# Kernel optimization log

Measured on AMD Instinct MI355X. Metric: run time of the kernel, lower is better.

## Reference

```python
import jax, jax.numpy as jnp
import numpy as np
from jax import lax

NUM_GROUPS = 16
EPS = 1e-5
POOL = 4
CLAMP_MIN, CLAMP_MAX = 0.0, 1.0


def setup_inputs() -> dict:
    key = jax.random.key(0)
    k = jax.random.split(key, 6)
    x = jax.random.normal(k[0], (128, 8, 128, 128), dtype=jnp.float32)
    conv_w = jax.random.normal(k[1], (64, 8, 3, 3), dtype=jnp.float32) * 0.1
    conv_b = jax.random.normal(k[2], (64,), dtype=jnp.float32) * 0.1
    gn_w = jnp.ones((64,), dtype=jnp.float32) + 0.1 * jax.random.normal(k[3], (64,), dtype=jnp.float32)
    gn_b = 0.1 * jax.random.normal(k[4], (64,), dtype=jnp.float32)
    scale = jnp.ones((64, 1, 1), dtype=jnp.float32) + 0.1 * jax.random.normal(k[5], (64, 1, 1), dtype=jnp.float32)
    return {"x": x, "conv_w": conv_w, "conv_b": conv_b, "gn_w": gn_w, "gn_b": gn_b, "scale": scale}


def reference(x, conv_w, conv_b, gn_w, gn_b, scale):
    # Conv2d: stride 1, no padding -> [N, 64, 126, 126]
    y = lax.conv_general_dilated(
        x, conv_w, window_strides=(1, 1), padding="VALID",
        dimension_numbers=("NCHW", "OIHW", "NCHW"))
    y = y + conv_b[None, :, None, None]

    # GroupNorm over (C/G, H, W) per (N, group), biased variance, eps=1e-5
    N, C, H, W = y.shape
    yg = y.reshape(N, NUM_GROUPS, -1)
    mean = jnp.mean(yg, axis=-1, keepdims=True)
    var = jnp.mean(jnp.square(yg - mean), axis=-1, keepdims=True)
    yn = ((yg - mean) * lax.rsqrt(var + EPS)).reshape(N, C, H, W)
    yn = yn * gn_w[None, :, None, None] + gn_b[None, :, None, None]

    # Per-channel scale (scale has shape [C,1,1])
    yn = yn * scale[None]

    # MaxPool2d(kernel=4, stride=4) -> [N, 64, 31, 31]
    yp = lax.reduce_window(yn, -jnp.inf, lax.max,
                           window_dimensions=(1, 1, POOL, POOL),
                           window_strides=(1, 1, POOL, POOL),
                           padding="VALID")

    # Clamp
    return jnp.clip(yp, CLAMP_MIN, CLAMP_MAX)
```

## Files before the change

kernel.cpp:

```cpp
#include <hip/hip_runtime.h>
#include <math.h>

#define N_IMG 128
#define IC 8
#define IH 128
#define IW 128
#define OC 64
#define NG 16
#define PH 31
#define PW 31
#define GN_EPS 1e-5f
#define CSTR (IH * IW)
#define NBAND 4

typedef float f32x4 __attribute__((ext_vector_type(4)));
typedef short s16x8 __attribute__((ext_vector_type(8)));
typedef int   i32x4 __attribute__((ext_vector_type(4)));

__device__ __forceinline__ unsigned cvt_pk_bf16(float a, float b) {
    unsigned r;
    asm("v_cvt_pk_bf16_f32 %0, %1, %2" : "=v"(r) : "v"(a), "v"(b));
    return r;
}
__device__ __forceinline__ float bf16lo_f(unsigned p) { return __uint_as_float(p << 16); }
__device__ __forceinline__ float bf16hi_f(unsigned p) { return __uint_as_float(p & 0xFFFF0000u); }

__device__ __forceinline__ s16x8 mk_frag(unsigned a, unsigned b, unsigned c, unsigned d) {
    union { i32x4 i; s16x8 s; } u;
    u.i = (i32x4){(int)a, (int)b, (int)c, (int)d};
    return u.s;
}

__device__ __forceinline__ void split8(const float v[8], s16x8* hi, s16x8* lo) {
    unsigned h[4], l[4];
#pragma unroll
    for (int e = 0; e < 4; e++) {
        float a = v[2 * e], b = v[2 * e + 1];
        unsigned hp = cvt_pk_bf16(a, b);
        float ra = a - bf16lo_f(hp);
        float rb = b - bf16hi_f(hp);
        h[e] = hp;
        l[e] = cvt_pk_bf16(ra, rb);
    }
    *hi = mk_frag(h[0], h[1], h[2], h[3]);
    *lo = mk_frag(l[0], l[1], l[2], l[3]);
}

__attribute__((amdgpu_waves_per_eu(2, 4)))
__launch_bounds__(256)
__global__ void conv_pool_mfma_phase1(const float* __restrict__ x,
                                      const float* __restrict__ conv_w,
                                      const float* __restrict__ conv_b,
                                      const float* __restrict__ gn_w,
                                      const float* __restrict__ gn_b,
                                      const float* __restrict__ scale,
                                      float* __restrict__ out,
                                      float* __restrict__ ws) {
    const int b = blockIdx.x;
    const int wid = ((b & 7) << 6) | (b >> 3);
    const int n = wid >> 2;
    const int band = wid & 3;
    const int tid = threadIdx.x;
    const int lane = tid & 63;
    const int wave = tid >> 6;
    const int p15 = lane & 15;
    const int lg = lane >> 4;

    __shared__ float gsum[4][NG][2];

    const float* xn = x + (size_t)n * (IC * CSTR);

    int icA[6], khA[6], rowoffA[6];
#pragma unroll
    for (int sh = 0; sh < 6; sh++) {
        int s = sh >> 1, h = sh & 1;
        int k0 = 32 * s + 16 * h + 4 * lg;
        int ic = k0 / 12;
        int kk = k0 - 12 * ic;
        int kh = kk >> 2;
        icA[sh] = ic; khA[sh] = kh;
        rowoffA[sh] = ic * CSTR + kh * IW;
    }

    s16x8 Ah[4][3], Al[4][3];
#pragma unroll
    for (int q = 0; q < 4; q++) {
        int c = q * 16 + p15;
        float sg = (gn_w[c] * scale[c] >= 0.f) ? 1.f : -1.f;
#pragma unroll
        for (int s = 0; s < 3; s++) {
            float wf[8];
#pragma unroll
            for (int h = 0; h < 2; h++) {
                int sh = s * 2 + h;
                int ic = icA[sh], kh = khA[sh];
#pragma unroll
                for (int kw = 0; kw < 4; kw++)
                    wf[h * 4 + kw] = (kw < 3)
                        ? conv_w[c * (IC * 9) + ic * 9 + kh * 3 + kw] * sg
                        : 0.f;
            }
            split8(wf, &Ah[q][s], &Al[q][s]);
        }
    }

    float bias4[4][4], sgn4[4][4];
#pragma unroll
    for (int q = 0; q < 4; q++)
#pragma unroll
        for (int r = 0; r < 4; r++) {
            int c = q * 16 + 4 * lg + r;
            float sg = (gn_w[c] * scale[c] >= 0.f) ? 1.f : -1.f;
            sgn4[q][r] = sg;
            bias4[q][r] = conv_b[c] * sg;
        }

    float sA[4], ssA[4];
#pragma unroll
    for (int q = 0; q < 4; q++) { sA[q] = 0.f; ssA[q] = 0.f; }

    const int nc = (band < 3) ? 8 * PW : 7 * PW;
    const int phb = band * 8;
    const int pi = p15 >> 2, pj = p15 & 3;

#pragma unroll 1
    for (int cell = wave; cell < nc; cell += 4) {
        int lph = cell / 31;
        int pwc = cell - lph * 31;
        int ph = phb + lph;
        int posoff = (4 * ph + pi) * IW + 4 * pwc + pj;

        f32x4 acc[4];
#pragma unroll
        for (int q = 0; q < 4; q++)
            acc[q] = (f32x4){bias4[q][0], bias4[q][1], bias4[q][2], bias4[q][3]};

#pragma unroll
        for (int s = 0; s < 3; s++) {
            float bv[8];
#pragma unroll
            for (int h = 0; h < 2; h++) {
                const float* p = xn + rowoffA[s * 2 + h] + posoff;
                bv[h * 4 + 0] = p[0]; bv[h * 4 + 1] = p[1];
                bv[h * 4 + 2] = p[2]; bv[h * 4 + 3] = p[3];
            }
            s16x8 Bh, Bl;
            split8(bv, &Bh, &Bl);
#pragma unroll
            for (int q = 0; q < 4; q++) {
                acc[q] = __builtin_amdgcn_mfma_f32_16x16x32_bf16(Ah[q][s], Bh, acc[q], 0, 0, 0);
                acc[q] = __builtin_amdgcn_mfma_f32_16x16x32_bf16(Ah[q][s], Bl, acc[q], 0, 0, 0);
                acc[q] = __builtin_amdgcn_mfma_f32_16x16x32_bf16(Al[q][s], Bh, acc[q], 0, 0, 0);
            }
        }

#pragma unroll
        for (int q = 0; q < 4; q++) {
            float m0 = acc[q][0], m1 = acc[q][1], m2 = acc[q][2], m3 = acc[q][3];
            float sp = sgn4[q][0] * m0 + sgn4[q][1] * m1
                     + sgn4[q][2] * m2 + sgn4[q][3] * m3;
            float sq = m0 * m0 + m1 * m1 + m2 * m2 + m3 * m3;
#pragma unroll
            for (int o = 1; o < 16; o <<= 1) {
                sp += __shfl_xor(sp, o, 64);
                sq += __shfl_xor(sq, o, 64);
                m0 = fmaxf(m0, __shfl_xor(m0, o, 64));
                m1 = fmaxf(m1, __shfl_xor(m1, o, 64));
                m2 = fmaxf(m2, __shfl_xor(m2, o, 64));
                m3 = fmaxf(m3, __shfl_xor(m3, o, 64));
            }
            sA[q] += sp; ssA[q] += sq;
            if (p15 == 0) {
                int c = q * 16 + 4 * lg;
                size_t ob = (((size_t)n * OC + c) * PH + ph) * PW + pwc;
                out[ob] = m0;
                out[ob + PH * PW] = m1;
                out[ob + 2 * PH * PW] = m2;
                out[ob + 3 * PH * PW] = m3;
            }
        }
    }

#pragma unroll 1
    for (int t = 2 * wave; t < 2 * wave + 2; t++) {
        int eb = band * 8 + t;
        int posrow, poscol, valid;
        if (eb < 16) {
            posrow = 8 * eb + (p15 >> 1);
            poscol = 124 + (p15 & 1);
            valid = (posrow <= 125);
        } else {
            posrow = 124 + (p15 >> 3);
            poscol = 8 * (eb - 16) + (p15 & 7);
            valid = (poscol <= 123);
        }

        f32x4 acc[4];
#pragma unroll
        for (int q = 0; q < 4; q++)
            acc[q] = (f32x4){bias4[q][0], bias4[q][1], bias4[q][2], bias4[q][3]};

#pragma unroll
        for (int s = 0; s < 3; s++) {
            float bv[8];
#pragma unroll
            for (int h = 0; h < 2; h++) {
                int sh = s * 2 + h;
                int xr = posrow + khA[sh]; if (xr > 127) xr = 127;
                const float* p = xn + icA[sh] * CSTR + xr * IW;
                int c0 = poscol;
                int c1 = c0 + 1; if (c1 > 127) c1 = 127;
                int c2 = c0 + 2; if (c2 > 127) c2 = 127;
                int c3 = c0 + 3; if (c3 > 127) c3 = 127;
                bv[h * 4 + 0] = p[c0]; bv[h * 4 + 1] = p[c1];
                bv[h * 4 + 2] = p[c2]; bv[h * 4 + 3] = p[c3];
            }
            s16x8 Bh, Bl;
            split8(bv, &Bh, &Bl);
#pragma unroll
            for (int q = 0; q < 4; q++) {
                acc[q] = __builtin_amdgcn_mfma_f32_16x16x32_bf16(Ah[q][s], Bh, acc[q], 0, 0, 0);
                acc[q] = __builtin_amdgcn_mfma_f32_16x16x32_bf16(Ah[q][s], Bl, acc[q], 0, 0, 0);
                acc[q] = __builtin_amdgcn_mfma_f32_16x16x32_bf16(Al[q][s], Bh, acc[q], 0, 0, 0);
            }
        }

        float vmask = valid ? 1.f : 0.f;
#pragma unroll
        for (int q = 0; q < 4; q++) {
            float m0 = acc[q][0] * vmask, m1 = acc[q][1] * vmask;
            float m2 = acc[q][2] * vmask, m3 = acc[q][3] * vmask;
            float sp = sgn4[q][0] * m0 + sgn4[q][1] * m1
                     + sgn4[q][2] * m2 + sgn4[q][3] * m3;
            float sq = m0 * m0 + m1 * m1 + m2 * m2 + m3 * m3;
#pragma unroll
            for (int o = 1; o < 16; o <<= 1) {
                sp += __shfl_xor(sp, o, 64);
                sq += __shfl_xor(sq, o, 64);
            }
            sA[q] += sp; ssA[q] += sq;
        }
    }

    if (p15 == 0) {
#pragma unroll
        for (int q = 0; q < 4; q++) {
            gsum[wave][q * 4 + lg][0] = sA[q];
            gsum[wave][q * 4 + lg][1] = ssA[q];
        }
    }
    __syncthreads();
    if (tid < 32) {
        int g = tid >> 1, which = tid & 1;
        float v = gsum[0][g][which] + gsum[1][g][which]
                + gsum[2][g][which] + gsum[3][g][which];
        ws[((size_t)(n * NBAND + band) * NG + g) * 2 + which] = v;
    }
}

__launch_bounds__(256)
__global__ void finalize_phase2(const float* __restrict__ gn_w,
                                const float* __restrict__ gn_b,
                                const float* __restrict__ scale,
                                const float* __restrict__ ws,
                                float* __restrict__ out) {
    const int total = N_IMG * OC * PH * PW;
    const float inv_count = 1.f / (float)(4 * 126 * 126);
    int stride = gridDim.x * 256;
    for (int i = blockIdx.x * 256 + threadIdx.x; i < total; i += stride) {
        int n = i / (OC * PH * PW);
        int rem = i - n * (OC * PH * PW);
        int c = rem / (PH * PW);
        int g = c >> 2;
        float S = 0.f, SS = 0.f;
#pragma unroll
        for (int bnd = 0; bnd < NBAND; bnd++) {
            size_t wb = ((size_t)(n * NBAND + bnd) * NG + g) * 2;
            S += ws[wb];
            SS += ws[wb + 1];
        }
        float mean = S * inv_count;
        float var = SS * inv_count - mean * mean;
        if (var < 0.f) var = 0.f;
        float rstd = rsqrtf(var + GN_EPS);
        float gw = gn_w[c], sc = scale[c];
        float a2 = rstd * fabsf(gw * sc);
        float b2 = (gn_b[c] - mean * rstd * gw) * sc;
        float v = fmaf(a2, out[i], b2);
        out[i] = fminf(fmaxf(v, 0.f), 1.f);
    }
}

extern "C" void kernel_launch(void* const* d_in, const int* in_sizes, int n_in,
                              void* d_out, int out_size, void* d_ws, size_t ws_size,
                              hipStream_t stream) {
    const float* x      = (const float*)d_in[0];
    const float* conv_w = (const float*)d_in[1];
    const float* conv_b = (const float*)d_in[2];
    const float* gn_w   = (const float*)d_in[3];
    const float* gn_b   = (const float*)d_in[4];
    const float* scale  = (const float*)d_in[5];
    float* out = (float*)d_out;
    float* ws  = (float*)d_ws;

    hipLaunchKernelGGL(conv_pool_mfma_phase1, dim3(N_IMG * NBAND), dim3(256),
                       0, stream, x, conv_w, conv_b, gn_w, gn_b, scale, out, ws);
    hipLaunchKernelGGL(finalize_phase2, dim3(2048), dim3(256), 0, stream,
                       gn_w, gn_b, scale, ws, out);
}
```

Measured before the change: 328.9 us.

## Map MFMA columns to pool windows so max-pool reduces in registers

Result: slower. 449.7 us (+36.7%).

```diff
diff --git a/kernel.cpp b/kernel.cpp
--- a/kernel.cpp
+++ b/kernel.cpp
@@ -119,80 +119,100 @@
 #pragma unroll
     for (int q = 0; q < 4; q++) { sA[q] = 0.f; ssA[q] = 0.f; }
 
-    const int nc = (band < 3) ? 8 * PW : 7 * PW;
+    const int ntile = (band < 3) ? 16 : 14;
     const int phb = band * 8;
-    const int pi = p15 >> 2, pj = p15 & 3;
 
 #pragma unroll 1
-    for (int cell = wave; cell < nc; cell += 4) {
-        int lph = cell / 31;
-        int pwc = cell - lph * 31;
-        int ph = phb + lph;
-        int posoff = (4 * ph + pi) * IW + 4 * pwc + pj;
-
-        f32x4 acc[4];
+    for (int t = wave; t < ntile; t += 4) {
+        const int ph = phb + (t >> 1);
+        const int tb = (t & 1) * 16;
+        const int pw = tb + p15;
+        const int valid = (pw <= 30);
+        const int pwc = valid ? pw : 30;
+        const float msk = valid ? 1.f : 0.f;
+        const float* xtile = xn + (4 * ph) * IW + 4 * pwc;
+
+        f32x4 vmax[4];
 #pragma unroll
         for (int q = 0; q < 4; q++)
-            acc[q] = (f32x4){bias4[q][0], bias4[q][1], bias4[q][2], bias4[q][3]};
-
-#pragma unroll
-        for (int s = 0; s < 3; s++) {
-            float bv[8];
-#pragma unroll
-            for (int h = 0; h < 2; h++) {
-                const float* p = xn + rowoffA[s * 2 + h] + posoff;
-                bv[h * 4 + 0] = p[0]; bv[h * 4 + 1] = p[1];
-                bv[h * 4 + 2] = p[2]; bv[h * 4 + 3] = p[3];
-            }
-            s16x8 Bh, Bl;
-            split8(bv, &Bh, &Bl);
-#pragma unroll
-            for (int q = 0; q < 4; q++) {
-                acc[q] = __builtin_amdgcn_mfma_f32_16x16x32_bf16(Ah[q][s], Bh, acc[q], 0, 0, 0);
-                acc[q] = __builtin_amdgcn_mfma_f32_16x16x32_bf16(Ah[q][s], Bl, acc[q], 0, 0, 0);
-                acc[q] = __builtin_amdgcn_mfma_f32_16x16x32_bf16(Al[q][s], Bh, acc[q], 0, 0, 0);
-            }
-        }
-
-#pragma unroll
-        for (int q = 0; q < 4; q++) {
-            float m0 = acc[q][0], m1 = acc[q][1], m2 = acc[q][2], m3 = acc[q][3];
-            float sp = sgn4[q][0] * m0 + sgn4[q][1] * m1
-                     + sgn4[q][2] * m2 + sgn4[q][3] * m3;
-            float sq = m0 * m0 + m1 * m1 + m2 * m2 + m3 * m3;
-#pragma unroll
-            for (int o = 1; o < 16; o <<= 1) {
-                sp += __shfl_xor(sp, o, 64);
-                sq += __shfl_xor(sq, o, 64);
-                m0 = fmaxf(m0, __shfl_xor(m0, o, 64));
-                m1 = fmaxf(m1, __shfl_xor(m1, o, 64));
-                m2 = fmaxf(m2, __shfl_xor(m2, o, 64));
-                m3 = fmaxf(m3, __shfl_xor(m3, o, 64));
-            }
-            sA[q] += sp; ssA[q] += sq;
-            if (p15 == 0) {
-                int c = q * 16 + 4 * lg;
-                size_t ob = (((size_t)n * OC + c) * PH + ph) * PW + pwc;
-                out[ob] = m0;
-                out[ob + PH * PW] = m1;
-                out[ob + 2 * PH * PW] = m2;
-                out[ob + 3 * PH * PW] = m3;
-            }
+            vmax[q] = (f32x4){-INFINITY, -INFINITY, -INFINITY, -INFINITY};
+
+#pragma unroll
+        for (int pi = 0; pi < 4; pi++) {
+            float row8[6][8];
+#pragma unroll
+            for (int sh = 0; sh < 6; sh++) {
+                const float* p = xtile + rowoffA[sh] + pi * IW;
+                float4 a = *(const float4*)p;
+                float4 bq = *(const float4*)(p + 4);
+                row8[sh][0] = a.x;  row8[sh][1] = a.y;
+                row8[sh][2] = a.z;  row8[sh][3] = a.w;
+                row8[sh][4] = bq.x; row8[sh][5] = bq.y;
+                row8[sh][6] = bq.z; row8[sh][7] = bq.w;
+            }
+#pragma unroll
+            for (int pj = 0; pj < 4; pj++) {
+                f32x4 acc[4];
+#pragma unroll
+                for (int q = 0; q < 4; q++)
+                    acc[q] = (f32x4){bias4[q][0], bias4[q][1],
+                                     bias4[q][2], bias4[q][3]};
+#pragma unroll
+                for (int s = 0; s < 3; s++) {
+                    float bv[8];
+#pragma unroll
+                    for (int h = 0; h < 2; h++)
+#pragma unroll
+                        for (int e = 0; e < 4; e++)
+                            bv[h * 4 + e] = row8[s * 2 + h][pj + e];
+                    s16x8 Bh, Bl;
+                    split8(bv, &Bh, &Bl);
+#pragma unroll
+                    for (int q = 0; q < 4; q++) {
+                        acc[q] = __builtin_amdgcn_mfma_f32_16x16x32_bf16(Ah[q][s], Bh, acc[q], 0, 0, 0);
+                        acc[q] = __builtin_amdgcn_mfma_f32_16x16x32_bf16(Ah[q][s], Bl, acc[q], 0, 0, 0);
+                        acc[q] = __builtin_amdgcn_mfma_f32_16x16x32_bf16(Al[q][s], Bh, acc[q], 0, 0, 0);
+                    }
+                }
+#pragma unroll
+                for (int q = 0; q < 4; q++) {
+                    float m0 = acc[q][0], m1 = acc[q][1];
+                    float m2 = acc[q][2], m3 = acc[q][3];
+                    vmax[q][0] = fmaxf(vmax[q][0], m0);
+                    vmax[q][1] = fmaxf(vmax[q][1], m1);
+                    vmax[q][2] = fmaxf(vmax[q][2], m2);
+                    vmax[q][3] = fmaxf(vmax[q][3], m3);
+                    float sp = sgn4[q][0] * m0 + sgn4[q][1] * m1
+                             + sgn4[q][2] * m2 + sgn4[q][3] * m3;
+                    float sq = m0 * m0 + m1 * m1 + m2 * m2 + m3 * m3;
+                    sA[q]  = fmaf(msk, sp, sA[q]);
+                    ssA[q] = fmaf(msk, sq, ssA[q]);
+                }
+            }
+        }
+        if (valid) {
+#pragma unroll
+            for (int q = 0; q < 4; q++)
+#pragma unroll
+                for (int r = 0; r < 4; r++) {
+                    int c = q * 16 + 4 * lg + r;
+                    out[(((size_t)n * OC + c) * PH + ph) * PW + pw] = vmax[q][r];
+                }
         }
     }
 
 #pragma unroll 1
     for (int t = 2 * wave; t < 2 * wave + 2; t++) {
         int eb = band * 8 + t;
-        int posrow, poscol, valid;
+        int posrow, poscol, evalid;
         if (eb < 16) {
             posrow = 8 * eb + (p15 >> 1);
             poscol = 124 + (p15 & 1);
-            valid = (posrow <= 125);
+            evalid = (posrow <= 125);
         } else {
             posrow = 124 + (p15 >> 3);
             poscol = 8 * (eb - 16) + (p15 & 7);
-            valid = (poscol <= 123);
+            evalid = (poscol <= 123);
         }
 
         f32x4 acc[4];
@@ -225,28 +245,28 @@
             }
         }
 
-        float vmask = valid ? 1.f : 0.f;
+        float vmask = evalid ? 1.f : 0.f;
 #pragma unroll
         for (int q = 0; q < 4; q++) {
             float m0 = acc[q][0] * vmask, m1 = acc[q][1] * vmask;
             float m2 = acc[q][2] * vmask, m3 = acc[q][3] * vmask;
-            float sp = sgn4[q][0] * m0 + sgn4[q][1] * m1
-                     + sgn4[q][2] * m2 + sgn4[q][3] * m3;
-            float sq = m0 * m0 + m1 * m1 + m2 * m2 + m3 * m3;
-#pragma unroll
-            for (int o = 1; o < 16; o <<= 1) {
-                sp += __shfl_xor(sp, o, 64);
-                sq += __shfl_xor(sq, o, 64);
-            }
-            sA[q] += sp; ssA[q] += sq;
-        }
-    }
-
-    if (p15 == 0) {
-#pragma unroll
-        for (int q = 0; q < 4; q++) {
-            gsum[wave][q * 4 + lg][0] = sA[q];
-            gsum[wave][q * 4 + lg][1] = ssA[q];
+            sA[q]  += sgn4[q][0] * m0 + sgn4[q][1] * m1
+                    + sgn4[q][2] * m2 + sgn4[q][3] * m3;
+            ssA[q] += m0 * m0 + m1 * m1 + m2 * m2 + m3 * m3;
+        }
+    }
+
+#pragma unroll
+    for (int q = 0; q < 4; q++) {
+        float sp = sA[q], sq = ssA[q];
+#pragma unroll
+        for (int o = 1; o < 16; o <<= 1) {
+            sp += __shfl_xor(sp, o, 64);
+            sq += __shfl_xor(sq, o, 64);
+        }
+        if (p15 == 0) {
+            gsum[wave][q * 4 + lg][0] = sp;
+            gsum[wave][q * 4 + lg][1] = sq;
         }
     }
     __syncthreads();
```
